# Kernel tuning notes

Measured on AMD Instinct MI355X. Metric: run time of the kernel, lower is better.

## Reference

```python
import jax, jax.numpy as jnp
import numpy as np

MODEL_DIM = 1024
HEAD_SIZE = 128

def setup_inputs() -> dict:
    key = jax.random.key(0)
    k0, k1, k2, k3 = jax.random.split(key, 4)
    embedded = jax.random.normal(k0, (4, 4096, MODEL_DIM), dtype=jnp.float32)
    # nn.Linear(model_dim, head_size, bias=False) weights: [head_size, model_dim]
    s = 1.0 / np.sqrt(MODEL_DIM)
    Wk = jax.random.uniform(k1, (HEAD_SIZE, MODEL_DIM), jnp.float32, -s, s)
    Wq = jax.random.uniform(k2, (HEAD_SIZE, MODEL_DIM), jnp.float32, -s, s)
    Wv = jax.random.uniform(k3, (HEAD_SIZE, MODEL_DIM), jnp.float32, -s, s)
    return {"embedded": embedded, "Wk": Wk, "Wq": Wq, "Wv": Wv}

def reference(embedded, Wk, Wq, Wv):
    # embedded: [b, s, m]; W*: [h, m]
    keys = jnp.einsum('bsm,hm->bsh', embedded, Wk)
    queries = jnp.einsum('bsm,hm->bsh', embedded, Wq)
    values = jnp.einsum('bsm,hm->bsh', embedded, Wv)
    h = keys.shape[-1]
    scores = jnp.einsum('bqh,bkh->bqk', queries, keys) / jnp.sqrt(jnp.float32(h))  # [b,s,s]
    s_len = keys.shape[1]
    causal = jnp.tril(jnp.ones((s_len, s_len), dtype=bool))
    scores = jnp.where(causal, scores, -jnp.inf)
    probs = jax.nn.softmax(scores, axis=-1)
    return jnp.einsum('bqk,bkh->bqh', probs, values)
```

## Files before the change

### kernel.cpp

```cpp
#include <hip/hip_runtime.h>
#include <hip/hip_bf16.h>


#define SEQ 4096
#define BATCH 4
#define HS 128
#define SLOTS_PB 128

typedef unsigned short u16;
typedef __bf16 bf16x8 __attribute__((ext_vector_type(8)));
typedef _Float16 f16x4 __attribute__((ext_vector_type(4)));
typedef float f32x4 __attribute__((ext_vector_type(4)));

__device__ __forceinline__ u16 f2bf(float f) {
    union { float f; unsigned u; } v; v.f = f;
    unsigned u = v.u;
    return (u16)((u + 0x7FFFu + ((u >> 16) & 1u)) >> 16);
}
__device__ __forceinline__ float bf2f(u16 u) {
    union { unsigned u; float f; } v; v.u = ((unsigned)u) << 16; return v.f;
}
__device__ __forceinline__ u16 f2h(float f) {
    union { _Float16 h; u16 u; } v; v.h = (_Float16)f; return v.u;
}
__device__ __forceinline__ void async_cp16(const void* g, void* l) {
    __builtin_amdgcn_global_load_lds(
        (const __attribute__((address_space(1))) unsigned int*)g,
        (__attribute__((address_space(3))) unsigned int*)l, 16, 0, 0);
}
__device__ __forceinline__ int nsplit_of(int Q) {
    return Q / 5 + 1 + (Q >= 23 ? 1 : 0);
}

__global__ __launch_bounds__(256) void wconv_kernel(
    const float* __restrict__ Wk, const float* __restrict__ Wq,
    const float* __restrict__ Wv, u16* __restrict__ Wt)
{
    const int g    = blockIdx.x * 256 + threadIdx.x;
    const int lane = g & 63;
    const int kf   = (g >> 6) & 1;
    const int kc   = (g >> 7) & 15;
    const int nt   = g >> 11;
    const int row  = nt * 16 + (lane & 15);
    const int k0   = kc * 64 + kf * 32 + (lane >> 4) * 8;
    const float* src = (row < 128) ? Wk : ((row < 256) ? Wq : Wv);
    const float scale = (row >= 128 && row < 256)
        ? 0.08838834764831845f * 1.4426950408889634f : 1.0f;
    const float4 v0 = *(const float4*)&src[(size_t)(row & 127) * 1024 + k0];
    const float4 v1 = *(const float4*)&src[(size_t)(row & 127) * 1024 + k0 + 4];
    ushort4 a, b;
    a.x = f2bf(v0.x * scale); a.y = f2bf(v0.y * scale);
    a.z = f2bf(v0.z * scale); a.w = f2bf(v0.w * scale);
    b.x = f2bf(v1.x * scale); b.y = f2bf(v1.y * scale);
    b.z = f2bf(v1.z * scale); b.w = f2bf(v1.w * scale);
    *(ushort4*)&Wt[(size_t)g * 8]     = a;
    *(ushort4*)&Wt[(size_t)g * 8 + 4] = b;
}

__global__ __launch_bounds__(512, 2) void qkv_kernel(
    const float* __restrict__ emb, const u16* __restrict__ Wt,
    u16* __restrict__ Qf, u16* __restrict__ Kf, u16* __restrict__ Vf)
{
    __shared__ union {
        struct {
            u16 E[2][64][40];
            u16 B[2][24][512];
        } s;
        u16 sOut[64][392];
    } sm;

    const int tid  = threadIdx.x;
    const int wv   = tid >> 6;
    const int lane = tid & 63;
    const int quad = lane >> 4;
    const int l16  = lane & 15;
    const int rg2  = wv >> 2;
    const int cg   = wv & 3;
    const int R0   = blockIdx.x * 64;

    const int arow = tid >> 3, ak = tid & 7;
    const float* abase = &emb[(size_t)(R0 + arow) * 1024 + ak * 4];
    const char* WtB = (const char*)Wt;

    f32x4 acc[2][6];
    #pragma unroll
    for (int rg = 0; rg < 2; rg++)
        #pragma unroll
        for (int j = 0; j < 6; j++) acc[rg][j] = (f32x4){0.f, 0.f, 0.f, 0.f};

#define LOADA(c) (*(const float4*)&abase[(size_t)(c) * 32])
#define WRITEA(bufi, v)                                                        \
    {                                                                          \
        ushort4 o;                                                             \
        o.x = f2bf((v).x); o.y = f2bf((v).y);                                  \
        o.z = f2bf((v).z); o.w = f2bf((v).w);                                  \
        *(ushort4*)&sm.s.E[bufi][arow][ak * 4] = o;                            \
    }
#define STAGEB(bufi, c)                                                        \
    {                                                                          \
        _Pragma("unroll")                                                      \
        for (int i = 0; i < 3; i++) {                                          \
            const int nt = wv * 3 + i;                                         \
            async_cp16(WtB + (size_t)(nt * 32 + (c)) * 1024 + lane * 16,       \
                       (void*)&sm.s.B[bufi][nt][0]);                           \
        }                                                                      \
    }
#define COMPUTE(bufi)                                                          \
    {                                                                          \
        bf16x8 a[2];                                                           \
        _Pragma("unroll")                                                      \
        for (int rg = 0; rg < 2; rg++)                                         \
            a[rg] = *(const bf16x8*)&sm.s.E[bufi][rg2 * 32 + rg * 16 + l16][quad * 8]; \
        _Pragma("unroll")                                                      \
        for (int j = 0; j < 6; j++) {                                          \
            const bf16x8 bfr = *(const bf16x8*)&sm.s.B[bufi][cg * 6 + j][lane * 8]; \
            _Pragma("unroll")                                                  \
            for (int rg = 0; rg < 2; rg++)                                     \
                acc[rg][j] = __builtin_amdgcn_mfma_f32_16x16x32_bf16(a[rg], bfr, acc[rg][j], 0, 0, 0); \
        }                                                                      \
    }
#define ITER(bufi, c)                                                          \
    {                                                                          \
        if ((c) < 31) STAGEB((bufi) ^ 1, (c) + 1);                             \
        float4 avn{};                                                          \
        if ((c) < 30) avn = LOADA((c) + 2);                                    \
        COMPUTE(bufi);                                                         \
        if ((c) < 31) WRITEA((bufi) ^ 1, av1);                                 \
        av1 = avn;                                                             \
        __syncthreads();                                                       \
    }

    float4 av1;
    {
        const float4 av0 = LOADA(0);
        av1 = LOADA(1);
        STAGEB(0, 0);
        WRITEA(0, av0);
        __syncthreads();
    }

    for (int cc = 0; cc < 16; cc++) {
        ITER(0, 2 * cc);
        ITER(1, 2 * cc + 1);
    }

    #pragma unroll
    for (int nt = 0; nt < 6; nt++) {
        const int col = cg * 96 + nt * 16 + l16;
        #pragma unroll
        for (int rg = 0; rg < 2; rg++) {
            const int rl = rg2 * 32 + rg * 16 + quad * 4;
            #pragma unroll
            for (int r = 0; r < 4; r++) {
                const float v = acc[rg][nt][r];
                sm.sOut[rl + r][col] = (col < 256) ? f2bf(v) : f2h(v);
            }
        }
    }
    __syncthreads();

    const int b  = R0 >> 12;
    const int s0 = R0 & 4095;
    #pragma unroll
    for (int i = 0; i < 2; i++) {
        const int g    = tid + i * 512;
        const int lg   = g & 63;
        const int kfp  = (g >> 6) & 3;
        const int k16l = (g >> 8) & 3;
        const int rl   = k16l * 16 + (lg & 15);
        const int cl   = kfp * 32 + (lg >> 4) * 8;
        const size_t base = (((size_t)(b * 256 + (s0 >> 4) + k16l) * 4 + kfp) * 64 + lg) * 8;
        *(uint4*)&Kf[base] = *(const uint4*)&sm.sOut[rl][cl];
        *(uint4*)&Qf[base] = *(const uint4*)&sm.sOut[rl][128 + cl];
    }
    #pragma unroll
    for (int i = 0; i < 4; i++) {
        const int g   = tid + i * 512;
        const int lg  = g & 63;
        const int ntl = (g >> 6) & 3;
        const int ht  = g >> 8;
        const int h   = ht * 16 + (lg & 15);
        const int kl  = ntl * 16 + ((lg >> 4) & 3) * 4;
        ushort4 o;
        o.x = sm.sOut[kl + 0][256 + h];
        o.y = sm.sOut[kl + 1][256 + h];
        o.z = sm.sOut[kl + 2][256 + h];
        o.w = sm.sOut[kl + 3][256 + h];
        const int t64 = s0 >> 6;
        const size_t base = ((((size_t)(b * 64 + t64) * 8 + ht) * 4 + ntl) * 64 + lg) * 4;
        *(ushort4*)&Vf[base] = o;
    }
#undef LOADA
#undef WRITEA
#undef STAGEB
#undef COMPUTE
#undef ITER
}

template<bool DIRECT>
__global__ __launch_bounds__(512, 4) void attn_kernel(
    const u16* __restrict__ Qf, const u16* __restrict__ Kf,
    const u16* __restrict__ Vf, u16* __restrict__ Opart,
    float* __restrict__ lpart, float* __restrict__ out)
{
    __shared__ u16 sT[2][16384];

    const int tid  = threadIdx.x;
    const int wv   = tid >> 6;
    const int lane = tid & 63;
    const int quad = lane >> 4;
    const int l16  = lane & 15;

    const int L    = blockIdx.x;
    const int b    = L & 3;
    const int slot = L >> 2;

    int Q = 0, sp = 0;
    if constexpr (DIRECT) {
        Q = slot; sp = 0;
    } else {
        int acc = 0;
        #pragma unroll 1
        for (int qq = 0; qq < 32; ++qq) {
            const int n = nsplit_of(qq);
            if (slot < acc + n) { Q = qq; sp = slot - acc; break; }
            acc += n;
        }
    }
    const int total = 2 * Q + 2;
    const int ns    = DIRECT ? 1 : nsplit_of(Q);
    const int kbeg  = DIRECT ? 0 : (sp * total) / ns;
    const int kend  = DIRECT ? total : ((sp + 1) * total) / ns;

    const int q0 = Q * 128;
    const size_t bS = (size_t)b * SEQ;

    const char* KbB = (const char*)(Kf + (size_t)b * 524288);
    const char* VbB = (const char*)(Vf + (size_t)b * 524288);

    bf16x8 qf[4];
    const int q16 = Q * 8 + wv;
    #pragma unroll
    for (int kf = 0; kf < 4; kf++)
        qf[kf] = *(const bf16x8*)&Qf[(((size_t)(b * 256 + q16) * 4 + kf) * 64 + lane) * 8];

    float rs0 = 0.f;
    f32x4 O[8];
    #pragma unroll
    for (int ht = 0; ht < 8; ht++) O[ht] = (f32x4){0.f, 0.f, 0.f, 0.f};

    const int qg0 = q0 + wv * 16 + l16;

    const int lseg = wv * 1024 + lane * 16;
#define STAGE(bufi, kt)                                                        \
    {                                                                          \
        const char* ks = KbB + (size_t)(kt) * 16384;                           \
        const char* vs = VbB + (size_t)(kt) * 16384;                           \
        char* lb = (char*)&sT[bufi][0] + wv * 1024;                            \
        _Pragma("unroll")                                                      \
        for (int i = 0; i < 2; i++)                                            \
            async_cp16(ks + i * 8192 + lseg, lb + i * 8192);                   \
        _Pragma("unroll")                                                      \
        for (int i = 0; i < 2; i++)                                            \
            async_cp16(vs + i * 8192 + lseg, lb + 16384 + i * 8192);           \
    }

    STAGE(0, kbeg);
    __syncthreads();

    int buf = 0;
    for (int kt = kbeg; kt < kend; ++kt) {
        const int kb = kt * 64;
        if (kt + 1 < kend) STAGE(buf ^ 1, kt + 1);

        const bool diag = (kt >= 2 * Q);
        f16x4 pf0[4];
        #pragma unroll
        for (int nt = 0; nt < 4; nt++) {
            f32x4 s0 = (f32x4){0.f, 0.f, 0.f, 0.f};
            __builtin_amdgcn_s_setprio(1);
            #pragma unroll
            for (int kf = 0; kf < 4; kf++) {
                const bf16x8 kfr = *(const bf16x8*)&sT[buf][((nt * 4 + kf) << 9) + lane * 8];
                s0 = __builtin_amdgcn_mfma_f32_16x16x32_bf16(kfr, qf[kf], s0, 0, 0, 0);
            }
            __builtin_amdgcn_s_setprio(0);
            if (diag) {
                #pragma unroll
                for (int r = 0; r < 4; r++) {
                    const int kg = kb + nt * 16 + quad * 4 + r;
                    if (kg > qg0) s0[r] = -3.0e38f;
                }
            }
            f16x4 p0;
            #pragma unroll
            for (int r = 0; r < 4; r++) {
                const float e0 = exp2f(s0[r] - 4.0f);
                rs0 += e0;
                p0[r] = (_Float16)e0;
            }
            pf0[nt] = p0;
        }

        __builtin_amdgcn_s_setprio(1);
        #pragma unroll
        for (int ht = 0; ht < 8; ht++) {
            f16x4 vf[4];
            #pragma unroll
            for (int nt = 0; nt < 4; nt++)
                vf[nt] = *(const f16x4*)&sT[buf][8192 + ((ht * 4 + nt) << 8) + lane * 4];
            #pragma unroll
            for (int nt = 0; nt < 4; nt++)
                O[ht] = __builtin_amdgcn_mfma_f32_16x16x16f16(vf[nt], pf0[nt], O[ht], 0, 0, 0);
        }
        __builtin_amdgcn_s_setprio(0);

        __syncthreads();
        buf ^= 1;
    }
#undef STAGE

    rs0 += __shfl_xor(rs0, 16); rs0 += __shfl_xor(rs0, 32);

    if constexpr (DIRECT) {
        const float inv = 1.0f / rs0;
        const int q = q0 + wv * 16 + l16;
        #pragma unroll
        for (int ht = 0; ht < 8; ht++) {
            f32x4 o = O[ht] * inv;
            *(f32x4*)&out[(bS + q) * HS + ht * 16 + quad * 4] = o;
        }
    } else {
        const size_t slotbase = (size_t)b * SLOTS_PB + slot;
        #pragma unroll
        for (int ht = 0; ht < 8; ht++) {
            const size_t j = ((slotbase * 8 + wv) * 8 + ht) * 64 + lane;
            ushort4 o;
            o.x = f2bf(O[ht][0]); o.y = f2bf(O[ht][1]);
            o.z = f2bf(O[ht][2]); o.w = f2bf(O[ht][3]);
            *(ushort4*)&Opart[j * 4] = o;
        }
        if (quad == 0)
            lpart[slotbase * 128 + wv * 16 + l16] = rs0;
    }
}

__global__ __launch_bounds__(256) void merge_kernel(
    const u16* __restrict__ Opart, const float* __restrict__ lpart,
    float* __restrict__ out)
{
    const int g  = blockIdx.x * 256 + threadIdx.x;
    const int b  = g >> 17;
    const int q  = (g >> 5) & 4095;
    const int hc = g & 31;
    const int Q  = q >> 7;
    const int ql = q & 127;
    const int wvv = ql >> 4, l16 = q & 15;
    const int ht = hc >> 2, qd = hc & 3;
    const int lane = qd * 16 + l16;

    int pre = 0, ns = 0;
    #pragma unroll 1
    for (int qq = 0; qq < 32; ++qq) {
        const int n = nsplit_of(qq);
        if (qq < Q) pre += n;
        else if (qq == Q) { ns = n; break; }
    }
    const size_t base_slot = (size_t)b * SLOTS_PB + pre;

    float den = 0.f;
    f32x4 num = (f32x4){0.f, 0.f, 0.f, 0.f};
    #pragma unroll 1
    for (int s = 0; s < ns; s++) {
        den += lpart[(base_slot + s) * 128 + ql];
        const size_t j = (((base_slot + s) * 8 + wvv) * 8 + ht) * 64 + lane;
        const ushort4 o = *(const ushort4*)&Opart[j * 4];
        num[0] += bf2f(o.x); num[1] += bf2f(o.y);
        num[2] += bf2f(o.z); num[3] += bf2f(o.w);
    }
    const float inv = 1.0f / den;
    float4 o; o.x = num[0] * inv; o.y = num[1] * inv;
    o.z = num[2] * inv; o.w = num[3] * inv;
    *(float4*)&out[(size_t)g * 4] = o;
}

extern "C" void kernel_launch(void* const* d_in, const int* in_sizes, int n_in,
                              void* d_out, int out_size, void* d_ws, size_t ws_size,
                              hipStream_t stream) {
    const float* emb = (const float*)d_in[0];
    const float* Wk  = (const float*)d_in[1];
    const float* Wq  = (const float*)d_in[2];
    const float* Wv  = (const float*)d_in[3];
    float* out = (float*)d_out;

    char* ws = (char*)d_ws;
    const size_t WBF_SZ    = (size_t)384 * 1024 * 2;
    const size_t QKV_SZ    = (size_t)BATCH * SEQ * HS * 2;
    const size_t Q_OFF     = WBF_SZ;
    const size_t K_OFF     = Q_OFF + QKV_SZ;
    const size_t V_OFF     = K_OFF + QKV_SZ;
    const size_t OPART_OFF = V_OFF + QKV_SZ;
    const size_t OPART_SZ  = (size_t)BATCH * SLOTS_PB * 32768;
    const size_t L_SZ      = (size_t)BATCH * SLOTS_PB * 128 * 4;

    u16* Wt = (u16*)ws;
    u16* Qf = (u16*)(ws + Q_OFF);
    u16* Kf = (u16*)(ws + K_OFF);
    u16* Vf = (u16*)(ws + V_OFF);

    wconv_kernel<<<dim3(192), dim3(256), 0, stream>>>(Wk, Wq, Wv, Wt);
    qkv_kernel<<<dim3(256), dim3(512), 0, stream>>>(emb, Wt, Qf, Kf, Vf);

    const size_t need = OPART_OFF + OPART_SZ + L_SZ;

    if (ws_size >= need) {
        u16*   Opart = (u16*)(ws + OPART_OFF);
        float* lp    = (float*)(ws + OPART_OFF + OPART_SZ);
        attn_kernel<false><<<dim3(4 * SLOTS_PB), dim3(512), 0, stream>>>(Qf, Kf, Vf, Opart, lp, out);
        merge_kernel<<<dim3(BATCH * SEQ * HS / 4 / 256), dim3(256), 0, stream>>>(Opart, lp, out);
    } else {
        attn_kernel<true><<<dim3(32 * BATCH), dim3(512), 0, stream>>>(Qf, Kf, Vf, nullptr, nullptr, out);
    }
}
```

Baseline: 165.6 us.

## Stage fp32 activations via async LDS loads in a 4-deep QKV pipeline

The QKV projection kernel now copies fp32 embedding tiles straight into LDS with global_load_lds, using an XOR swizzle to avoid bank conflicts, instead of going through registers and converting to bf16 before the LDS write. The bf16 conversion moves into the compute step after the LDS read. The single-stage double buffer with __syncthreads becomes a 4-buffer ring with 3 stages in flight, synchronized by vmcnt waits plus a barrier. This is meant to hide global-load latency and free registers, at the cost of more LDS (4x24x512 u16 plus 4x64x32 floats, about 130KB), which may cut occupancy below the 2 blocks per CU the launch bounds ask for.

Result: slower. 190.7 us (+15.2%).

```diff
diff --git a/kernel.cpp b/kernel.cpp
--- a/kernel.cpp
+++ b/kernel.cpp
@@ -22,6 +22,9 @@
 }
 __device__ __forceinline__ u16 f2h(float f) {
     union { _Float16 h; u16 u; } v; v.h = (_Float16)f; return v.u;
+}
+__device__ __forceinline__ __bf16 f2bfh(float f) {
+    union { unsigned short u; __bf16 h; } v; v.u = f2bf(f); return v.h;
 }
 __device__ __forceinline__ void async_cp16(const void* g, void* l) {
     __builtin_amdgcn_global_load_lds(
@@ -63,8 +66,8 @@
 {
     __shared__ union {
         struct {
-            u16 E[2][64][40];
-            u16 B[2][24][512];
+            u16   B[4][24][512];
+            float A[4][64][32];
         } s;
         u16 sOut[64][392];
     } sm;
@@ -78,8 +81,9 @@
     const int cg   = wv & 3;
     const int R0   = blockIdx.x * 64;
 
-    const int arow = tid >> 3, ak = tid & 7;
-    const float* abase = &emb[(size_t)(R0 + arow) * 1024 + ak * 4];
+    const int arow = tid >> 3;
+    const int aslot = (tid & 7) ^ ((tid >> 3) & 7);
+    const float* asrc = &emb[(size_t)(R0 + arow) * 1024 + aslot * 4];
     const char* WtB = (const char*)Wt;
 
     f32x4 acc[2][6];
@@ -88,29 +92,42 @@
         #pragma unroll
         for (int j = 0; j < 6; j++) acc[rg][j] = (f32x4){0.f, 0.f, 0.f, 0.f};
 
-#define LOADA(c) (*(const float4*)&abase[(size_t)(c) * 32])
-#define WRITEA(bufi, v)                                                        \
+#define STAGE(c)                                                               \
     {                                                                          \
-        ushort4 o;                                                             \
-        o.x = f2bf((v).x); o.y = f2bf((v).y);                                  \
-        o.z = f2bf((v).z); o.w = f2bf((v).w);                                  \
-        *(ushort4*)&sm.s.E[bufi][arow][ak * 4] = o;                            \
-    }
-#define STAGEB(bufi, c)                                                        \
-    {                                                                          \
+        const int bufi = (c) & 3;                                              \
         _Pragma("unroll")                                                      \
         for (int i = 0; i < 3; i++) {                                          \
             const int nt = wv * 3 + i;                                         \
             async_cp16(WtB + (size_t)(nt * 32 + (c)) * 1024 + lane * 16,       \
                        (void*)&sm.s.B[bufi][nt][0]);                           \
         }                                                                      \
-    }
-#define COMPUTE(bufi)                                                          \
+        async_cp16((const void*)(asrc + (c) * 32),                             \
+                   (void*)&sm.s.A[bufi][wv * 8][0]);                           \
+    }
+#define WAITBAR(N)                                                             \
     {                                                                          \
+        asm volatile("s_waitcnt vmcnt(" #N ")" ::: "memory");                  \
+        __builtin_amdgcn_sched_barrier(0);                                     \
+        __builtin_amdgcn_s_barrier();                                          \
+        __builtin_amdgcn_sched_barrier(0);                                     \
+    }
+#define COMPUTE(c)                                                             \
+    {                                                                          \
+        const int bufi = (c) & 3;                                              \
         bf16x8 a[2];                                                           \
         _Pragma("unroll")                                                      \
-        for (int rg = 0; rg < 2; rg++)                                         \
-            a[rg] = *(const bf16x8*)&sm.s.E[bufi][rg2 * 32 + rg * 16 + l16][quad * 8]; \
+        for (int rg = 0; rg < 2; rg++) {                                       \
+            const int r  = rg2 * 32 + rg * 16 + l16;                           \
+            const int sw = (l16 & 7) << 2;          \
+            const f32x4 lo = *(const f32x4*)&sm.s.A[bufi][r][(quad * 8 + 0) ^ sw]; \
+            const f32x4 hi = *(const f32x4*)&sm.s.A[bufi][r][(quad * 8 + 4) ^ sw]; \
+            bf16x8 av;                                                         \
+            av[0] = f2bfh(lo[0]); av[1] = f2bfh(lo[1]);                        \
+            av[2] = f2bfh(lo[2]); av[3] = f2bfh(lo[3]);                        \
+            av[4] = f2bfh(hi[0]); av[5] = f2bfh(hi[1]);                        \
+            av[6] = f2bfh(hi[2]); av[7] = f2bfh(hi[3]);                        \
+            a[rg] = av;                                                        \
+        }                                                                      \
         _Pragma("unroll")                                                      \
         for (int j = 0; j < 6; j++) {                                          \
             const bf16x8 bfr = *(const bf16x8*)&sm.s.B[bufi][cg * 6 + j][lane * 8]; \
@@ -119,30 +136,19 @@
                 acc[rg][j] = __builtin_amdgcn_mfma_f32_16x16x32_bf16(a[rg], bfr, acc[rg][j], 0, 0, 0); \
         }                                                                      \
     }
-#define ITER(bufi, c)                                                          \
-    {                                                                          \
-        if ((c) < 31) STAGEB((bufi) ^ 1, (c) + 1);                             \
-        float4 avn{};                                                          \
-        if ((c) < 30) avn = LOADA((c) + 2);                                    \
-        COMPUTE(bufi);                                                         \
-        if ((c) < 31) WRITEA((bufi) ^ 1, av1);                                 \
-        av1 = avn;                                                             \
-        __syncthreads();                                                       \
-    }
-
-    float4 av1;
-    {
-        const float4 av0 = LOADA(0);
-        av1 = LOADA(1);
-        STAGEB(0, 0);
-        WRITEA(0, av0);
-        __syncthreads();
-    }
-
-    for (int cc = 0; cc < 16; cc++) {
-        ITER(0, 2 * cc);
-        ITER(1, 2 * cc + 1);
-    }
+
+    STAGE(0);
+    STAGE(1);
+    STAGE(2);
+    for (int c = 0; c < 29; c++) {
+        WAITBAR(8);
+        STAGE(c + 3);
+        COMPUTE(c);
+    }
+    WAITBAR(8); COMPUTE(29);
+    WAITBAR(4); COMPUTE(30);
+    WAITBAR(0); COMPUTE(31);
+    __syncthreads();
 
     #pragma unroll
     for (int nt = 0; nt < 6; nt++) {
@@ -190,11 +196,9 @@
         const size_t base = ((((size_t)(b * 64 + t64) * 8 + ht) * 4 + ntl) * 64 + lg) * 4;
         *(ushort4*)&Vf[base] = o;
     }
-#undef LOADA
-#undef WRITEA
-#undef STAGEB
+#undef STAGE
+#undef WAITBAR
 #undef COMPUTE
-#undef ITER
 }
 
 template<bool DIRECT>
```
